# Optimization experiments

Hardware: AMD Instinct MI355X
Metric: run time of the kernel (lower is better)

Reference implementation:

```python
import jax, jax.numpy as jnp
import numpy as np

N_REFLNS = 2_000_000
N_IMAGES = 8192
N_RAC = 1_000_000
MC = 8
D_META = 16
HIDDEN = 32
LOG_2PI = 1.8378770664093453


def setup_inputs() -> dict:
    key = jax.random.key(0)
    ks = jax.random.split(key, 12)
    return {
        'q_loc': jax.random.normal(ks[0], (N_RAC,), jnp.float32),
        'q_log_scale': 0.1 * jax.random.normal(ks[1], (N_RAC,), jnp.float32) - 1.0,
        'eps': jax.random.normal(ks[2], (MC, N_RAC), jnp.float32),
        'metadata': jax.random.normal(ks[3], (N_REFLNS, D_META), jnp.float32),
        'W1': jax.random.normal(ks[4], (D_META, HIDDEN), jnp.float32) / np.sqrt(D_META),
        'b1': jnp.zeros((HIDDEN,), jnp.float32),
        'W2': jax.random.normal(ks[5], (HIDDEN, MC), jnp.float32) / np.sqrt(HIDDEN),
        'b2': jnp.zeros((MC,), jnp.float32),
        'iobs': jax.random.normal(ks[6], (N_REFLNS,), jnp.float32),
        'sigiobs': jax.random.uniform(ks[7], (N_REFLNS,), jnp.float32) + 0.1,  # positive std
        'image_id': jnp.sort(jax.random.randint(ks[8], (N_REFLNS,), 0, N_IMAGES)),
        'miller_id': jax.random.randint(ks[9], (N_REFLNS,), 0, N_RAC),
    }


def average_by_images(ll, image_id):
    # scatter_add per image, summed over MC samples, then normalized
    per_img = jax.ops.segment_sum(ll.sum(axis=1), image_id, num_segments=N_IMAGES)
    counts = jax.ops.segment_sum(jnp.ones((ll.shape[0],), ll.dtype), image_id, num_segments=N_IMAGES)
    return per_img / jnp.maximum(counts, 1.0) / ll.shape[1]


def reference(q_loc, q_log_scale, eps, metadata, W1, b1, W2, b2, iobs, sigiobs, image_id, miller_id):
    q_scale = jnp.exp(q_log_scale)
    # reparameterized MC samples from surrogate posterior: (MC, N_RAC)
    z = q_loc + q_scale * eps
    # analytic KL( N(loc, scale) || N(0, 1) ) per RAC entry
    kl = 0.5 * (q_scale * q_scale + q_loc * q_loc - 1.0) - q_log_scale
    # scale model: positive per-(refln, sample) scale from metadata
    h = jax.nn.relu(metadata @ W1 + b1)
    scale = jax.nn.softplus(h @ W2 + b2)                # (N_REFLNS, MC)
    # rac.gather: per-reflection structure factor samples
    f = jnp.take(z.T, miller_id, axis=0)                # (N_REFLNS, MC)
    ipred = f * f * scale
    # Normal log-likelihood of iobs given ipred, std sigiobs
    resid = (ipred - iobs[:, None]) / sigiobs[:, None]
    ll = -0.5 * resid * resid - jnp.log(sigiobs)[:, None] - 0.5 * LOG_2PI
    ll_img = average_by_images(ll, image_id)            # (N_IMAGES,)
    ipred_avg = ipred.mean(axis=-1)                     # (N_REFLNS,)
    return ipred_avg, -ll_img.mean(), kl.mean()
```

## Files before the change

kernel.cpp:

```cpp
#include <hip/hip_runtime.h>
#include <hip/hip_bf16.h>
#include <math.h>

#define N_REFLNS 2000000
#define N_IMAGES 8192
#define N_RAC    1000000
#define MC       8
#define D_META   16
#define HIDDEN   32
#define LOG_2PI  1.8378770664093453f
#define LOG2E    1.44269504089f
#define LN2      0.69314718056f


typedef __attribute__((ext_vector_type(8)))  short bf16x8;
typedef __attribute__((ext_vector_type(4)))  float f32x4;
typedef __attribute__((ext_vector_type(16))) float f32x16;

#define MFMA16(A, B, C) __builtin_amdgcn_mfma_f32_16x16x32_bf16(A, B, C, 0, 0, 0)
#define MFMA32(A, B, C) __builtin_amdgcn_mfma_f32_32x32x16_bf16(A, B, C, 0, 0, 0)

union B8 { bf16x8 v; unsigned u[4]; };

__device__ __forceinline__ void split_hilo(const float* x, bf16x8& hi, bf16x8& lo) {
    B8 h, l;
    #pragma unroll
    for (int p = 0; p < 4; p++) {
        unsigned u0 = __float_as_uint(x[2 * p]);
        unsigned u1 = __float_as_uint(x[2 * p + 1]);
        unsigned hf0 = u0 & 0xFFFF0000u;
        unsigned hf1 = u1 & 0xFFFF0000u;
        h.u[p] = (u0 >> 16) | hf1;
        float d0 = x[2 * p]     - __uint_as_float(hf0);
        float d1 = x[2 * p + 1] - __uint_as_float(hf1);
        l.u[p] = (__float_as_uint(d0) >> 16) | (__float_as_uint(d1) & 0xFFFF0000u);
    }
    hi = h.v; lo = l.v;
}

__device__ __forceinline__ bf16x8 pack8_rne(float4 a0, float4 a1) {
    B8 r;
    __hip_bfloat162 t0 = __float22bfloat162_rn(make_float2(a0.x, a0.y));
    __hip_bfloat162 t1 = __float22bfloat162_rn(make_float2(a0.z, a0.w));
    __hip_bfloat162 t2 = __float22bfloat162_rn(make_float2(a1.x, a1.y));
    __hip_bfloat162 t3 = __float22bfloat162_rn(make_float2(a1.z, a1.w));
    r.u[0] = reinterpret_cast<unsigned&>(t0);
    r.u[1] = reinterpret_cast<unsigned&>(t1);
    r.u[2] = reinterpret_cast<unsigned&>(t2);
    r.u[3] = reinterpret_cast<unsigned&>(t3);
    return r.v;
}

__device__ __forceinline__ float softplus_fast(float x) {
    float t = __builtin_amdgcn_exp2f(-fabsf(x) * LOG2E);
    return fmaxf(x, 0.0f) + LN2 * __builtin_amdgcn_logf(1.0f + t);
}

__global__ __launch_bounds__(256) void k_z_kl(
    const float* __restrict__ q_loc,
    const float* __restrict__ q_log_scale,
    const float* __restrict__ eps,
    float* __restrict__ zT,
    float* __restrict__ kl_sum)
{
    int t = blockIdx.x * 256 + threadIdx.x;
    int r0 = t * 4;
    float kl = 0.0f;
    if (r0 < N_RAC) {
        float4 ql  = *(const float4*)(q_loc + r0);
        float4 qls = *(const float4*)(q_log_scale + r0);
        float4 qs;
        qs.x = expf(qls.x); qs.y = expf(qls.y);
        qs.z = expf(qls.z); qs.w = expf(qls.w);
        kl = 0.5f * (qs.x * qs.x + ql.x * ql.x - 1.0f) - qls.x
           + 0.5f * (qs.y * qs.y + ql.y * ql.y - 1.0f) - qls.y
           + 0.5f * (qs.z * qs.z + ql.z * ql.z - 1.0f) - qls.z
           + 0.5f * (qs.w * qs.w + ql.w * ql.w - 1.0f) - qls.w;
        if (zT) {
            float zr[4][MC];
            #pragma unroll
            for (int s = 0; s < MC; s++) {
                float4 e = *(const float4*)(eps + (size_t)s * N_RAC + r0);
                zr[0][s] = ql.x + qs.x * e.x;
                zr[1][s] = ql.y + qs.y * e.y;
                zr[2][s] = ql.z + qs.z * e.z;
                zr[3][s] = ql.w + qs.w * e.w;
            }
            #pragma unroll
            for (int r = 0; r < 4; r++) {
                float4* dst = (float4*)(zT + (size_t)(r0 + r) * MC);
                dst[0] = make_float4(zr[r][0], zr[r][1], zr[r][2], zr[r][3]);
                dst[1] = make_float4(zr[r][4], zr[r][5], zr[r][6], zr[r][7]);
            }
        }
    }
    __shared__ float sred[256];
    sred[threadIdx.x] = kl;
    __syncthreads();
    #pragma unroll
    for (int s = 128; s > 0; s >>= 1) {
        if (threadIdx.x < s) sred[threadIdx.x] += sred[threadIdx.x + s];
        __syncthreads();
    }
    if (threadIdx.x == 0) atomicAdd(kl_sum, sred[0]);
}

template <bool HAS_Z>
__global__ __launch_bounds__(256) void k_main(
    const float* __restrict__ metadata,
    const float* __restrict__ W1, const float* __restrict__ b1,
    const float* __restrict__ W2, const float* __restrict__ b2,
    const float* __restrict__ iobs, const float* __restrict__ sigiobs,
    const int* __restrict__ image_id, const int* __restrict__ miller_id,
    const float* __restrict__ zT,
    const float* __restrict__ q_loc, const float* __restrict__ q_log_scale,
    const float* __restrict__ eps,
    float* __restrict__ out_ipred,
    float* __restrict__ img_sum, float* __restrict__ img_cnt)
{
    __shared__ __align__(16) float sH[4][32 * 36];
    __shared__ __align__(16) float sL[4][4 * 160];
    __shared__ int   s_id[256];
    __shared__ float s_ll[256];
    __shared__ float s_ct[256];

    int tid  = threadIdx.x;
    int wave = tid >> 6;
    int lane = tid & 63;
    int n31  = lane & 31;
    int kh   = lane >> 5;
    int q    = lane >> 4;
    int c16  = lane & 15;

    bf16x8 W1h, W1l;
    {
        float tmp[8];
        #pragma unroll
        for (int j = 0; j < 8; j++) tmp[j] = W1[(kh * 8 + j) * HIDDEN + n31];
        split_hilo(tmp, W1h, W1l);
    }
    float b1v = b1[n31];

    bf16x8 W2h, W2l;
    {
        float tmp[8];
        #pragma unroll
        for (int j = 0; j < 8; j++) tmp[j] = (c16 < MC) ? W2[(q * 8 + j) * MC + c16] : 0.0f;
        split_hilo(tmp, W2h, W2l);
    }
    float b2v = (c16 < MC) ? b2[c16] : 0.0f;

    int base_w = blockIdx.x * 256 + wave * 64;
    float* Hb = &sH[wave][0];
    float* Lb = &sL[wave][0];

    #pragma unroll
    for (int st = 0; st < 2; st++) {
        int rowbase = base_w + st * 32;
        int r = rowbase + n31;
        if (r > N_REFLNS - 1) r = N_REFLNS - 1;
        const float4* mp = (const float4*)(metadata + (size_t)r * D_META + kh * 8);
        float4 a0 = mp[0], a1 = mp[1];
        float av[8] = {a0.x, a0.y, a0.z, a0.w, a1.x, a1.y, a1.z, a1.w};
        bf16x8 Ah, Al;
        split_hilo(av, Ah, Al);

        f32x16 cc;
        #pragma unroll
        for (int i = 0; i < 16; i++) cc[i] = b1v;
        cc = MFMA32(Al, W1h, cc);
        cc = MFMA32(Ah, W1l, cc);
        cc = MFMA32(Ah, W1h, cc);
        #pragma unroll
        for (int i = 0; i < 16; i++) {
            int row = (i & 3) + 8 * (i >> 2) + 4 * kh;
            Hb[row * 36 + n31] = fmaxf(cc[i], 0.0f);
        }

        #pragma unroll
        for (int t2 = 0; t2 < 2; t2++) {
            const float4* hp = (const float4*)(Hb + (t2 * 16 + c16) * 36 + q * 8);
            bf16x8 Hh = pack8_rne(hp[0], hp[1]);
            f32x4 c2 = {b2v, b2v, b2v, b2v};
            c2 = MFMA16(Hh, W2l, c2);
            c2 = MFMA16(Hh, W2h, c2);
            if (c16 < MC) {
                #pragma unroll
                for (int rr = 0; rr < 4; rr++) {
                    Lb[(st * 2 + t2) * 160 + (q * 4 + rr) * 10 + c16] = c2[rr];
                }
            }
        }
    }

    int n = base_w + lane;
    bool valid = (n < N_REFLNS);
    float ll_sum = 0.0f;
    int img = -1;

    if (valid) {
        float lg[MC];
        {
            const float2* lp = (const float2*)(Lb + (lane >> 4) * 160 + c16 * 10);
            float2 p0 = lp[0], p1 = lp[1], p2 = lp[2], p3 = lp[3];
            lg[0] = p0.x; lg[1] = p0.y; lg[2] = p1.x; lg[3] = p1.y;
            lg[4] = p2.x; lg[5] = p2.y; lg[6] = p3.x; lg[7] = p3.y;
        }
        int m = miller_id[n];
        float io = iobs[n];
        float sg = sigiobs[n];
        img = image_id[n];

        float f[MC];
        if (HAS_Z) {
            const float4* zp = (const float4*)(zT + (size_t)m * MC);
            float4 z0 = zp[0], z1 = zp[1];
            f[0] = z0.x; f[1] = z0.y; f[2] = z0.z; f[3] = z0.w;
            f[4] = z1.x; f[5] = z1.y; f[6] = z1.z; f[7] = z1.w;
        } else {
            float qlv = q_loc[m];
            float qsv = expf(q_log_scale[m]);
            #pragma unroll
            for (int s = 0; s < MC; s++) f[s] = qlv + qsv * eps[(size_t)s * N_RAC + m];
        }

        float sum_ip = 0.0f, sum_d2 = 0.0f;
        #pragma unroll
        for (int s = 0; s < MC; s++) {
            float sc = softplus_fast(lg[s]);
            float ip = f[s] * f[s] * sc;
            sum_ip += ip;
            float d = ip - io;
            sum_d2 = fmaf(d, d, sum_d2);
        }
        float inv = __builtin_amdgcn_rcpf(sg);
        out_ipred[n] = sum_ip * (1.0f / MC);
        ll_sum = -0.5f * sum_d2 * inv * inv
                 - (float)MC * (0.5f * LOG_2PI)
                 - (float)MC * (LN2 * __builtin_amdgcn_logf(sg));
    }

    s_ll[tid] = ll_sum;
    s_ct[tid] = valid ? 1.0f : 0.0f;
    s_id[tid] = img;
    __syncthreads();
    #pragma unroll
    for (int d = 1; d < 256; d <<= 1) {
        float a = 0.0f, c = 0.0f;
        if (tid >= d && s_id[tid] == s_id[tid - d]) {
            a = s_ll[tid - d];
            c = s_ct[tid - d];
        }
        __syncthreads();
        s_ll[tid] += a;
        s_ct[tid] += c;
        __syncthreads();
    }
    if (valid) {
        bool tail = (tid == 255) || (s_id[tid + 1] != img);
        if (tail) {
            atomicAdd(&img_sum[img], s_ll[tid]);
            atomicAdd(&img_cnt[img], s_ct[tid]);
        }
    }
}

__global__ __launch_bounds__(256) void k_final(
    const float* __restrict__ img_sum,
    const float* __restrict__ img_cnt,
    const float* __restrict__ kl_sum,
    float* __restrict__ out)
{
    __shared__ float sred[256];
    float acc = 0.0f;
    for (int i = threadIdx.x; i < N_IMAGES; i += 256) {
        acc += img_sum[i] / fmaxf(img_cnt[i], 1.0f);
    }
    sred[threadIdx.x] = acc;
    __syncthreads();
    #pragma unroll
    for (int s = 128; s > 0; s >>= 1) {
        if (threadIdx.x < s) sred[threadIdx.x] += sred[threadIdx.x + s];
        __syncthreads();
    }
    if (threadIdx.x == 0) {
        float mean_ll = sred[0] / ((float)MC * (float)N_IMAGES);
        out[N_REFLNS]     = -mean_ll;
        out[N_REFLNS + 1] = kl_sum[0] * (1.0f / (float)N_RAC);
    }
}

extern "C" void kernel_launch(void* const* d_in, const int* in_sizes, int n_in,
                              void* d_out, int out_size, void* d_ws, size_t ws_size,
                              hipStream_t stream) {
    const float* q_loc       = (const float*)d_in[0];
    const float* q_log_scale = (const float*)d_in[1];
    const float* eps         = (const float*)d_in[2];
    const float* metadata    = (const float*)d_in[3];
    const float* W1          = (const float*)d_in[4];
    const float* b1          = (const float*)d_in[5];
    const float* W2          = (const float*)d_in[6];
    const float* b2          = (const float*)d_in[7];
    const float* iobs        = (const float*)d_in[8];
    const float* sigiobs     = (const float*)d_in[9];
    const int*   image_id    = (const int*)d_in[10];
    const int*   miller_id   = (const int*)d_in[11];
    float* out = (float*)d_out;

    char* ws = (char*)d_ws;
    float* img_sum = (float*)ws;
    float* img_cnt = img_sum + N_IMAGES;
    float* kl_sum  = img_cnt + N_IMAGES;
    const size_t z_off = 65664;
    bool has_z = (ws_size >= z_off + (size_t)N_RAC * MC * sizeof(float));
    float* zT = has_z ? (float*)(ws + z_off) : nullptr;

    hipMemsetAsync(d_ws, 0, (2 * N_IMAGES + 1) * sizeof(float), stream);

    k_z_kl<<<(N_RAC / 4 + 255) / 256, 256, 0, stream>>>(q_loc, q_log_scale, eps, zT, kl_sum);

    if (has_z) {
        k_main<true><<<(N_REFLNS + 255) / 256, 256, 0, stream>>>(
            metadata, W1, b1, W2, b2, iobs, sigiobs, image_id, miller_id,
            zT, q_loc, q_log_scale, eps, out, img_sum, img_cnt);
    } else {
        k_main<false><<<(N_REFLNS + 255) / 256, 256, 0, stream>>>(
            metadata, W1, b1, W2, b2, iobs, sigiobs, image_id, miller_id,
            nullptr, q_loc, q_log_scale, eps, out, img_sum, img_cnt);
    }

    k_final<<<1, 256, 0, stream>>>(img_sum, img_cnt, kl_sum, out);
}
```

Baseline: 292.3 us.

## Replace block LDS segmented scan with wave shuffle scan and hoist gathers

The per-image segmented reduction moves from a shared-memory scan with many block-wide barriers to a wave-level shuffle scan, with one atomic per image segment per wave. The per-reflection loads (miller_id, iobs, sigiobs, image_id, the zT gather and metadata) are issued at kernel start, so their latency overlaps the MLP work. The trade-off is roughly four times as many global atomics (one per wave rather than one per block) and more live registers. The z/kl kernel also swaps expf for a hardware exp2-based exponent.

```diff
diff --git a/kernel.cpp b/kernel.cpp
--- a/kernel.cpp
+++ b/kernel.cpp
@@ -70,8 +70,10 @@
         float4 ql  = *(const float4*)(q_loc + r0);
         float4 qls = *(const float4*)(q_log_scale + r0);
         float4 qs;
-        qs.x = expf(qls.x); qs.y = expf(qls.y);
-        qs.z = expf(qls.z); qs.w = expf(qls.w);
+        qs.x = __builtin_amdgcn_exp2f(qls.x * LOG2E);
+        qs.y = __builtin_amdgcn_exp2f(qls.y * LOG2E);
+        qs.z = __builtin_amdgcn_exp2f(qls.z * LOG2E);
+        qs.w = __builtin_amdgcn_exp2f(qls.w * LOG2E);
         kl = 0.5f * (qs.x * qs.x + ql.x * ql.x - 1.0f) - qls.x
            + 0.5f * (qs.y * qs.y + ql.y * ql.y - 1.0f) - qls.y
            + 0.5f * (qs.z * qs.z + ql.z * ql.z - 1.0f) - qls.z
@@ -120,9 +122,6 @@
 {
     __shared__ __align__(16) float sH[4][32 * 36];
     __shared__ __align__(16) float sL[4][4 * 160];
-    __shared__ int   s_id[256];
-    __shared__ float s_ll[256];
-    __shared__ float s_ct[256];
 
     int tid  = threadIdx.x;
     int wave = tid >> 6;
@@ -132,6 +131,38 @@
     int q    = lane >> 4;
     int c16  = lane & 15;
 
+    int base_w = blockIdx.x * 256 + wave * 64;
+
+    int n = base_w + lane;
+    bool valid = (n < N_REFLNS);
+    int nc = valid ? n : (N_REFLNS - 1);
+    int m    = miller_id[nc];
+    float io = iobs[nc];
+    float sg = sigiobs[nc];
+    int img  = image_id[nc];
+    float f[MC];
+    if (HAS_Z) {
+        const float4* zp = (const float4*)(zT + (size_t)m * MC);
+        float4 z0 = zp[0], z1 = zp[1];
+        f[0] = z0.x; f[1] = z0.y; f[2] = z0.z; f[3] = z0.w;
+        f[4] = z1.x; f[5] = z1.y; f[6] = z1.z; f[7] = z1.w;
+    } else {
+        float qlv = q_loc[m];
+        float qsv = expf(q_log_scale[m]);
+        #pragma unroll
+        for (int s = 0; s < MC; s++) f[s] = qlv + qsv * eps[(size_t)s * N_RAC + m];
+    }
+
+    float4 a_m[2][2];
+    #pragma unroll
+    for (int st = 0; st < 2; st++) {
+        int r = base_w + st * 32 + n31;
+        if (r > N_REFLNS - 1) r = N_REFLNS - 1;
+        const float4* mp = (const float4*)(metadata + (size_t)r * D_META + kh * 8);
+        a_m[st][0] = mp[0];
+        a_m[st][1] = mp[1];
+    }
+
     bf16x8 W1h, W1l;
     {
         float tmp[8];
@@ -140,7 +171,6 @@
         split_hilo(tmp, W1h, W1l);
     }
     float b1v = b1[n31];
-
     bf16x8 W2h, W2l;
     {
         float tmp[8];
@@ -150,17 +180,12 @@
     }
     float b2v = (c16 < MC) ? b2[c16] : 0.0f;
 
-    int base_w = blockIdx.x * 256 + wave * 64;
     float* Hb = &sH[wave][0];
     float* Lb = &sL[wave][0];
 
     #pragma unroll
     for (int st = 0; st < 2; st++) {
-        int rowbase = base_w + st * 32;
-        int r = rowbase + n31;
-        if (r > N_REFLNS - 1) r = N_REFLNS - 1;
-        const float4* mp = (const float4*)(metadata + (size_t)r * D_META + kh * 8);
-        float4 a0 = mp[0], a1 = mp[1];
+        float4 a0 = a_m[st][0], a1 = a_m[st][1];
         float av[8] = {a0.x, a0.y, a0.z, a0.w, a1.x, a1.y, a1.z, a1.w};
         bf16x8 Ah, Al;
         split_hilo(av, Ah, Al);
@@ -193,36 +218,13 @@
         }
     }
 
-    int n = base_w + lane;
-    bool valid = (n < N_REFLNS);
     float ll_sum = 0.0f;
-    int img = -1;
-
-    if (valid) {
+    {
         float lg[MC];
-        {
-            const float2* lp = (const float2*)(Lb + (lane >> 4) * 160 + c16 * 10);
-            float2 p0 = lp[0], p1 = lp[1], p2 = lp[2], p3 = lp[3];
-            lg[0] = p0.x; lg[1] = p0.y; lg[2] = p1.x; lg[3] = p1.y;
-            lg[4] = p2.x; lg[5] = p2.y; lg[6] = p3.x; lg[7] = p3.y;
-        }
-        int m = miller_id[n];
-        float io = iobs[n];
-        float sg = sigiobs[n];
-        img = image_id[n];
-
-        float f[MC];
-        if (HAS_Z) {
-            const float4* zp = (const float4*)(zT + (size_t)m * MC);
-            float4 z0 = zp[0], z1 = zp[1];
-            f[0] = z0.x; f[1] = z0.y; f[2] = z0.z; f[3] = z0.w;
-            f[4] = z1.x; f[5] = z1.y; f[6] = z1.z; f[7] = z1.w;
-        } else {
-            float qlv = q_loc[m];
-            float qsv = expf(q_log_scale[m]);
-            #pragma unroll
-            for (int s = 0; s < MC; s++) f[s] = qlv + qsv * eps[(size_t)s * N_RAC + m];
-        }
+        const float2* lp = (const float2*)(Lb + (lane >> 4) * 160 + c16 * 10);
+        float2 p0 = lp[0], p1 = lp[1], p2 = lp[2], p3 = lp[3];
+        lg[0] = p0.x; lg[1] = p0.y; lg[2] = p1.x; lg[3] = p1.y;
+        lg[4] = p2.x; lg[5] = p2.y; lg[6] = p3.x; lg[7] = p3.y;
 
         float sum_ip = 0.0f, sum_d2 = 0.0f;
         #pragma unroll
@@ -234,34 +236,27 @@
             sum_d2 = fmaf(d, d, sum_d2);
         }
         float inv = __builtin_amdgcn_rcpf(sg);
-        out_ipred[n] = sum_ip * (1.0f / MC);
+        if (valid) out_ipred[n] = sum_ip * (1.0f / MC);
         ll_sum = -0.5f * sum_d2 * inv * inv
                  - (float)MC * (0.5f * LOG_2PI)
                  - (float)MC * (LN2 * __builtin_amdgcn_logf(sg));
     }
 
-    s_ll[tid] = ll_sum;
-    s_ct[tid] = valid ? 1.0f : 0.0f;
-    s_id[tid] = img;
-    __syncthreads();
-    #pragma unroll
-    for (int d = 1; d < 256; d <<= 1) {
-        float a = 0.0f, c = 0.0f;
-        if (tid >= d && s_id[tid] == s_id[tid - d]) {
-            a = s_ll[tid - d];
-            c = s_ct[tid - d];
-        }
-        __syncthreads();
-        s_ll[tid] += a;
-        s_ct[tid] += c;
-        __syncthreads();
-    }
-    if (valid) {
-        bool tail = (tid == 255) || (s_id[tid + 1] != img);
-        if (tail) {
-            atomicAdd(&img_sum[img], s_ll[tid]);
-            atomicAdd(&img_cnt[img], s_ct[tid]);
-        }
+    float v = valid ? ll_sum : 0.0f;
+    float c = valid ? 1.0f : 0.0f;
+    int   id = img;
+    #pragma unroll
+    for (int d = 1; d < 64; d <<= 1) {
+        float pv = __shfl_up(v, d, 64);
+        float pc = __shfl_up(c, d, 64);
+        int  pid = __shfl_up(id, d, 64);
+        if (lane >= d && pid == id) { v += pv; c += pc; }
+    }
+    int nid = __shfl_down(id, 1, 64);
+    bool tail = (lane == 63) || (nid != id);
+    if (valid && tail && c > 0.0f) {
+        atomicAdd(&img_sum[id], v);
+        atomicAdd(&img_cnt[id], c);
     }
 }
 
```

After: 287.9 us. Within noise of the previous version (-1.5%).
